# Optimization experiments

Hardware: AMD Instinct MI355X
Metric: run time of the kernel (lower is better)

Reference implementation:

```python
import jax, jax.numpy as jnp
import numpy as np
from jax import lax

B, D, BOND, OUT = 16384, 784, 5, 10

def setup_inputs() -> dict:
    key = jax.random.key(0)
    k = jax.random.split(key, 6)
    x = jax.random.uniform(k[0], (B, D), dtype=jnp.float32)
    core_first = jax.random.normal(k[1], (1, 2, BOND), dtype=jnp.float32) * 0.1
    cores_mid = jax.random.normal(k[2], (D - 2, BOND, 2, BOND), dtype=jnp.float32) * 0.1
    core_last = jax.random.normal(k[3], (BOND, 2, 1), dtype=jnp.float32) * 0.1
    # xavier_uniform for fc.weight with fan_in=1, fan_out=OUT
    bound = float(np.sqrt(6.0 / (1 + OUT)))
    fc_w = jax.random.uniform(k[4], (OUT, 1), dtype=jnp.float32, minval=-bound, maxval=bound)
    fc_b = jnp.zeros((OUT,), dtype=jnp.float32)
    return {"x": x, "core_first": core_first, "cores_mid": cores_mid,
            "core_last": core_last, "fc_w": fc_w, "fc_b": fc_b}

def reference(x, core_first, cores_mid, core_last, fc_w, fc_b):
    # x: [B, D] -> feature map [B, D, 2] = stack(1-x, x)
    xs = jnp.stack([1.0 - x, x], axis=-1)            # [B, D, 2]
    # first core: (1, 2, bond) -> initial carry [B, bond]
    carry0 = jnp.einsum('bi,ir->br', xs[:, 0], core_first[0])  # [B, bond]
    # sequential tensor-train contraction over middle sites via scan
    xs_mid = jnp.moveaxis(xs[:, 1:-1], 1, 0)          # [D-2, B, 2]
    def step(carry, inp):
        xi, core = inp                                # xi: [B,2], core: [bond,2,bond]
        carry = jnp.einsum('bl,bi,lir->br', carry, xi, core)
        return carry, None
    carry, _ = lax.scan(step, carry0, (xs_mid, cores_mid))
    # last core: (bond, 2, 1) -> scalar per batch element
    vlast = jnp.einsum('bi,li->bl', xs[:, -1], core_last[:, :, 0])  # [B, bond]
    res = jnp.sum(carry * vlast, axis=-1, keepdims=True)            # [B, 1]
    out = res @ fc_w.T + fc_b                          # [B, OUT]
    return out
```

## Files before the change

### kernel.cpp

```cpp
#include <hip/hip_runtime.h>


typedef float v4f __attribute__((ext_vector_type(4)));
typedef float v2f __attribute__((ext_vector_type(2)));

constexpr int Bn     = 16384;
constexpr int Dn     = 784;
constexpr int NOUT   = 10;
constexpr int NPAIR  = 390;
constexpr int PVEC   = 15;
constexpr int PMAT   = 12;
constexpr int RHP0   = 195;
constexpr int BWD_P0 = 375;
constexpr int PAIR_F = 100;
constexpr int WROFF  = Bn * 5;

__device__ __forceinline__ v4f splat4(float x) { v4f v = {x, x, x, x}; return v; }
__device__ __forceinline__ v4f fma4(v4f a, v4f b, v4f c) {
    return __builtin_elementwise_fma(a, b, c);
}

struct Frag { v4f r[5]; float c4[5]; };

__device__ __forceinline__ void matstepLM(const Frag& M, Frag& T,
                                          const float* __restrict__ s, v2f xc) {
    const float xa = xc[0], xb = xc[1], xab = xa * xb;
    const v4f va = splat4(xa), vb = splat4(xb), vp = splat4(xab);
    const v4f* s4 = (const v4f*)s;
#pragma unroll
    for (int l = 0; l < 5; ++l) {
        v4f crow = fma4(vp, s4[15 + l], fma4(vb, s4[10 + l], fma4(va, s4[5 + l], s4[l])));
        v4f cq = (l < 4) ? s4[20 + l] : s4[24];
        float c4l = fmaf(xab, cq[3], fmaf(xb, cq[2], fmaf(xa, cq[1], cq[0])));
#pragma unroll
        for (int i = 0; i < 5; ++i) {
            float mil = (l < 4) ? M.r[i][l] : M.c4[i];
            if (l == 0) {
                T.r[i]  = splat4(mil) * crow;
                T.c4[i] = mil * c4l;
            } else {
                T.r[i]  = fma4(splat4(mil), crow, T.r[i]);
                T.c4[i] = fmaf(mil, c4l, T.c4[i]);
            }
        }
    }
}

__device__ __forceinline__ void vecstepLM(v4f& cv, float& c4,
                                          const float* __restrict__ s, v2f xc) {
    const float xa = xc[0], xb = xc[1], xab = xa * xb;
    const v4f va = splat4(xa), vb = splat4(xb), vp = splat4(xab);
    const v4f* s4 = (const v4f*)s;
    v4f acc; float a4;
#pragma unroll
    for (int l = 0; l < 5; ++l) {
        v4f crow = fma4(vp, s4[15 + l], fma4(vb, s4[10 + l], fma4(va, s4[5 + l], s4[l])));
        v4f cq = (l < 4) ? s4[20 + l] : s4[24];
        float c4l = fmaf(xab, cq[3], fmaf(xb, cq[2], fmaf(xa, cq[1], cq[0])));
        float cl = (l < 4) ? cv[l] : c4;
        if (l == 0) { acc = splat4(cl) * crow; a4 = cl * c4l; }
        else        { acc = fma4(splat4(cl), crow, acc); a4 = fmaf(cl, c4l, a4); }
    }
    cv = acc; c4 = a4;
}

__global__ void prepack_pairs(const float* __restrict__ cm, float* __restrict__ pk)
{
    int idx = blockIdx.x * 256 + threadIdx.x;
    if (idx >= NPAIR * 100) return;
    int p = idx / 100, rest = idx - p * 100;
    int q = rest / 25, e = rest - q * 25;
    int l = e / 5, r = e - l * 5;
    int m1 = 2 * p + 1, m2 = 2 * p + 2;
    const float* L = cm + (size_t)(m1 * 5 + l) * 10;
    float acc = 0.f;
#pragma unroll
    for (int k = 0; k < 5; ++k) {
        float Lk = (q & 1) ? (L[5 + k] - L[k]) : L[k];
        const float* R = cm + (size_t)(m2 * 5 + k) * 10;
        float Rk = (q & 2) ? (R[5 + r] - R[r]) : R[r];
        acc = fmaf(Lk, Rk, acc);
    }
    int wl = l, wr = r;
    if (p >= BWD_P0) { wl = r; wr = l; }
    int off;
    if (wr < 4)      off = q * 20 + wl * 4 + wr;
    else if (wl < 4) off = 80 + wl * 4 + q;
    else             off = 96 + q;
    pk[(size_t)p * PAIR_F + off] = acc;
}

__global__ __launch_bounds__(1024, 4)
void mps_half_kernel(const float* __restrict__ x,
                     const float* __restrict__ core_first,
                     const float* __restrict__ cores_mid,
                     const float* __restrict__ core_last,
                     const float* __restrict__ pk,
                     float* __restrict__ out)
{
    __shared__ float matbuf[8][25][64];

    const int lane = threadIdx.x & 63;
    const int wave = threadIdx.x >> 6;
    const int wu   = __builtin_amdgcn_readfirstlane(wave);
    const int g    = blockIdx.x >> 1;
    const int h    = blockIdx.x & 1;
    const int row  = g * 64 + lane;
    const float* __restrict__ xr = x + (size_t)row * Dn;
    const v2f* __restrict__ xr2 = (const v2f*)xr;

    if (wu >= 1) {
        const int p0 = (h == 0 ? PVEC : RHP0) + PMAT * (wu - 1);

        Frag M, T;
        M.r[0] = {1,0,0,0}; M.r[1] = {0,1,0,0}; M.r[2] = {0,0,1,0};
        M.r[3] = {0,0,0,1}; M.r[4] = {0,0,0,0};
        M.c4[0] = 0; M.c4[1] = 0; M.c4[2] = 0; M.c4[3] = 0; M.c4[4] = 1;

        v2f x0 = xr2[p0 + 1], x1 = xr2[p0 + 2];
#pragma unroll 1
        for (int j = 0; j < PMAT; j += 2) {
            const float* s0 = pk + (size_t)(p0 + j) * PAIR_F;
            v2f nx0 = xr2[p0 + j + 3], nx1 = xr2[p0 + j + 4];
            matstepLM(M, T, s0, x0);
            matstepLM(T, M, s0 + PAIR_F, x1);
            x0 = nx0; x1 = nx1;
        }

        const bool ph1 = (h == 0) ? (wu <= 8) : (wu >= 8);
        const int  k   = (h == 0) ? (ph1 ? wu - 1 : wu - 9)
                                  : (ph1 ? 15 - wu : 7 - wu);
        if (ph1) {
#pragma unroll
            for (int i = 0; i < 5; ++i) {
#pragma unroll
                for (int r = 0; r < 4; ++r) matbuf[k][i * 5 + r][lane] = M.r[i][r];
                matbuf[k][i * 5 + 4][lane] = M.c4[i];
            }
        }
        __syncthreads();
        __syncthreads();
        if (!ph1) {
#pragma unroll
            for (int i = 0; i < 5; ++i) {
#pragma unroll
                for (int r = 0; r < 4; ++r) matbuf[k][i * 5 + r][lane] = M.r[i][r];
                matbuf[k][i * 5 + 4][lane] = M.c4[i];
            }
        }
        __syncthreads();
    } else if (h == 0) {
        v2f x01 = xr2[0];
        float cl[5], cn[5];
#pragma unroll
        for (int r = 0; r < 5; ++r)
            cl[r] = fmaf(x01[0], core_first[5 + r] - core_first[r], core_first[r]);
        const float* cm0 = cores_mid;
#pragma unroll
        for (int r = 0; r < 5; ++r) {
            float a = 0.f;
#pragma unroll
            for (int l = 0; l < 5; ++l) {
                float m = fmaf(x01[1], cm0[l * 10 + 5 + r] - cm0[l * 10 + r], cm0[l * 10 + r]);
                a = fmaf(cl[l], m, a);
            }
            cn[r] = a;
        }
        v4f cv = {cn[0], cn[1], cn[2], cn[3]};
        float c4 = cn[4];

        v2f xc = xr2[1];
#pragma unroll 1
        for (int p = 0; p < PVEC; ++p) {
            v2f nx = xr2[p + 2];
            vecstepLM(cv, c4, pk + (size_t)p * PAIR_F, xc);
            xc = nx;
        }
        cl[0] = cv[0]; cl[1] = cv[1]; cl[2] = cv[2]; cl[3] = cv[3]; cl[4] = c4;

        __syncthreads();
#pragma unroll 1
        for (int k = 0; k < 8; ++k) {
            float v0[5];
#pragma unroll
            for (int r = 0; r < 5; ++r) v0[r] = cl[0] * matbuf[k][r][lane];
#pragma unroll
            for (int l = 1; l < 5; ++l)
#pragma unroll
                for (int r = 0; r < 5; ++r)
                    v0[r] = fmaf(cl[l], matbuf[k][l * 5 + r][lane], v0[r]);
#pragma unroll
            for (int r = 0; r < 5; ++r) cl[r] = v0[r];
        }
        __syncthreads();
        __syncthreads();
#pragma unroll 1
        for (int k = 0; k < 7; ++k) {
            float v0[5];
#pragma unroll
            for (int r = 0; r < 5; ++r) v0[r] = cl[0] * matbuf[k][r][lane];
#pragma unroll
            for (int l = 1; l < 5; ++l)
#pragma unroll
                for (int r = 0; r < 5; ++r)
                    v0[r] = fmaf(cl[l], matbuf[k][l * 5 + r][lane], v0[r]);
#pragma unroll
            for (int r = 0; r < 5; ++r) cl[r] = v0[r];
        }
        float* o = out + (size_t)row * 5;
#pragma unroll
        for (int i = 0; i < 5; ++i) o[i] = cl[i];
    } else {
        v2f xz = xr2[391];
        float vl[5], vn[5];
#pragma unroll
        for (int l = 0; l < 5; ++l)
            vl[l] = fmaf(xz[1], core_last[2 * l + 1] - core_last[2 * l], core_last[2 * l]);
        const float* cmL = cores_mid + (size_t)781 * 50;
#pragma unroll
        for (int l = 0; l < 5; ++l) {
            float a = 0.f;
#pragma unroll
            for (int r = 0; r < 5; ++r) {
                float m = fmaf(xz[0], cmL[l * 10 + 5 + r] - cmL[l * 10 + r], cmL[l * 10 + r]);
                a = fmaf(m, vl[r], a);
            }
            vn[l] = a;
        }
        v4f cv = {vn[0], vn[1], vn[2], vn[3]};
        float c4 = vn[4];

        v2f xc = xr2[390];
#pragma unroll 1
        for (int p = 389; p >= BWD_P0; --p) {
            v2f nx = xr2[p];
            vecstepLM(cv, c4, pk + (size_t)p * PAIR_F, xc);
            xc = nx;
        }
        float u[5] = {cv[0], cv[1], cv[2], cv[3], c4};

        __syncthreads();
#pragma unroll 1
        for (int k = 0; k < 8; ++k) {
            float v0[5];
#pragma unroll
            for (int i = 0; i < 5; ++i) {
                float a = matbuf[k][i * 5][lane] * u[0];
#pragma unroll
                for (int l = 1; l < 5; ++l)
                    a = fmaf(matbuf[k][i * 5 + l][lane], u[l], a);
                v0[i] = a;
            }
#pragma unroll
            for (int i = 0; i < 5; ++i) u[i] = v0[i];
        }
        __syncthreads();
        __syncthreads();
#pragma unroll 1
        for (int k = 0; k < 7; ++k) {
            float v0[5];
#pragma unroll
            for (int i = 0; i < 5; ++i) {
                float a = matbuf[k][i * 5][lane] * u[0];
#pragma unroll
                for (int l = 1; l < 5; ++l)
                    a = fmaf(matbuf[k][i * 5 + l][lane], u[l], a);
                v0[i] = a;
            }
#pragma unroll
            for (int i = 0; i < 5; ++i) u[i] = v0[i];
        }
        float* o = out + WROFF + (size_t)row * 5;
#pragma unroll
        for (int i = 0; i < 5; ++i) o[i] = u[i];
    }
}

__global__ __launch_bounds__(256)
void finish_dot(const float* __restrict__ outF, float* __restrict__ res)
{
    int r = blockIdx.x * 256 + threadIdx.x;
    const float* vl = outF + (size_t)r * 5;
    const float* wr = outF + WROFF + (size_t)r * 5;
    float s = vl[0] * wr[0];
#pragma unroll
    for (int i = 1; i < 5; ++i) s = fmaf(vl[i], wr[i], s);
    res[r] = s;
}

__global__ __launch_bounds__(256)
void finish_out(const float* __restrict__ res, const float* __restrict__ fc_w,
                const float* __restrict__ fc_b, float* __restrict__ out)
{
    int r = blockIdx.x * 256 + threadIdx.x;
    float rv = res[r];
    float* o = out + (size_t)r * NOUT;
#pragma unroll
    for (int j = 0; j < NOUT; ++j) o[j] = fmaf(rv, fc_w[j], fc_b[j]);
}

extern "C" void kernel_launch(void* const* d_in, const int* in_sizes, int n_in,
                              void* d_out, int out_size, void* d_ws, size_t ws_size,
                              hipStream_t stream) {
    const float* x          = (const float*)d_in[0];
    const float* core_first = (const float*)d_in[1];
    const float* cores_mid  = (const float*)d_in[2];
    const float* core_last  = (const float*)d_in[3];
    const float* fc_w       = (const float*)d_in[4];
    const float* fc_b       = (const float*)d_in[5];
    float* out              = (float*)d_out;
    float* pk               = (float*)d_ws;
    float* res              = (float*)d_ws;

    hipLaunchKernelGGL(prepack_pairs, dim3((NPAIR * 100 + 255) / 256), dim3(256),
                       0, stream, cores_mid, pk);
    hipLaunchKernelGGL(mps_half_kernel, dim3(512), dim3(1024), 0, stream,
                       x, core_first, cores_mid, core_last, pk, out);
    hipLaunchKernelGGL(finish_dot, dim3(Bn / 256), dim3(256), 0, stream,
                       out, res);
    hipLaunchKernelGGL(finish_out, dim3(Bn / 256), dim3(256), 0, stream,
                       res, fc_w, fc_b, out);
}
```

Measured before the change: 128.9 us.

## Stage half of pair-core data in LDS and shrink matrix exchange buffer

Each block now copies the first 40 floats (the constant and xa terms) of every pair core for its half of the chain into shared memory, while the xb and xab terms are still read from global memory. The buffer used to hand 5x5 segment matrices to the vector wave shrinks from 8 to 5 slots, and the exchange becomes three phases with extra barriers. The aim is to cut global/scalar memory traffic and to use less LDS for the matrix buffer. In exchange it adds a cooperative preload with a block-wide barrier at kernel start, more synchronisation phases, and about 31 KB of extra LDS for the core copy, which may limit how many blocks fit per CU.

```diff
diff --git a/kernel.cpp b/kernel.cpp
--- a/kernel.cpp
+++ b/kernel.cpp
@@ -22,15 +22,16 @@
 
 struct Frag { v4f r[5]; float c4[5]; };
 
-__device__ __forceinline__ void matstepLM(const Frag& M, Frag& T,
-                                          const float* __restrict__ s, v2f xc) {
+__device__ __forceinline__ void matstepH(const Frag& M, Frag& T,
+                                         const v4f* __restrict__ lq,
+                                         const float* __restrict__ g, v2f xc) {
     const float xa = xc[0], xb = xc[1], xab = xa * xb;
     const v4f va = splat4(xa), vb = splat4(xb), vp = splat4(xab);
-    const v4f* s4 = (const v4f*)s;
+    const v4f* g4 = (const v4f*)g;
 #pragma unroll
     for (int l = 0; l < 5; ++l) {
-        v4f crow = fma4(vp, s4[15 + l], fma4(vb, s4[10 + l], fma4(va, s4[5 + l], s4[l])));
-        v4f cq = (l < 4) ? s4[20 + l] : s4[24];
+        v4f crow = fma4(vp, g4[5 + l], fma4(vb, g4[l], fma4(va, lq[5 + l], lq[l])));
+        v4f cq = (l < 4) ? g4[10 + l] : g4[14];
         float c4l = fmaf(xab, cq[3], fmaf(xb, cq[2], fmaf(xa, cq[1], cq[0])));
 #pragma unroll
         for (int i = 0; i < 5; ++i) {
@@ -46,16 +47,17 @@
     }
 }
 
-__device__ __forceinline__ void vecstepLM(v4f& cv, float& c4,
-                                          const float* __restrict__ s, v2f xc) {
+__device__ __forceinline__ void vecstepH(v4f& cv, float& c4,
+                                         const v4f* __restrict__ lq,
+                                         const float* __restrict__ g, v2f xc) {
     const float xa = xc[0], xb = xc[1], xab = xa * xb;
     const v4f va = splat4(xa), vb = splat4(xb), vp = splat4(xab);
-    const v4f* s4 = (const v4f*)s;
+    const v4f* g4 = (const v4f*)g;
     v4f acc; float a4;
 #pragma unroll
     for (int l = 0; l < 5; ++l) {
-        v4f crow = fma4(vp, s4[15 + l], fma4(vb, s4[10 + l], fma4(va, s4[5 + l], s4[l])));
-        v4f cq = (l < 4) ? s4[20 + l] : s4[24];
+        v4f crow = fma4(vp, g4[5 + l], fma4(vb, g4[l], fma4(va, lq[5 + l], lq[l])));
+        v4f cq = (l < 4) ? g4[10 + l] : g4[14];
         float c4l = fmaf(xab, cq[3], fmaf(xb, cq[2], fmaf(xa, cq[1], cq[0])));
         float cl = (l < 4) ? cv[l] : c4;
         if (l == 0) { acc = splat4(cl) * crow; a4 = cl * c4l; }
@@ -98,19 +100,28 @@
                      const float* __restrict__ pk,
                      float* __restrict__ out)
 {
-    __shared__ float matbuf[8][25][64];
+    __shared__ v4f   pklds[195 * 10];
+    __shared__ float matbuf[5][25][64];
 
     const int lane = threadIdx.x & 63;
     const int wave = threadIdx.x >> 6;
     const int wu   = __builtin_amdgcn_readfirstlane(wave);
     const int g    = blockIdx.x >> 1;
     const int h    = blockIdx.x & 1;
+    const int p0g  = (h == 0) ? 0 : RHP0;
     const int row  = g * 64 + lane;
     const float* __restrict__ xr = x + (size_t)row * Dn;
     const v2f* __restrict__ xr2 = (const v2f*)xr;
+    const v4f* __restrict__ pk4 = (const v4f*)pk;
+
+    for (int t = threadIdx.x; t < 195 * 10; t += 1024) {
+        int pr = t / 10, q = t - pr * 10;
+        pklds[t] = pk4[(size_t)(p0g + pr) * 25 + q];
+    }
+    __syncthreads();
 
     if (wu >= 1) {
-        const int p0 = (h == 0 ? PVEC : RHP0) + PMAT * (wu - 1);
+        const int p0 = p0g + PVEC + PMAT * (wu - 1);
 
         Frag M, T;
         M.r[0] = {1,0,0,0}; M.r[1] = {0,1,0,0}; M.r[2] = {0,0,1,0};
@@ -120,17 +131,18 @@
         v2f x0 = xr2[p0 + 1], x1 = xr2[p0 + 2];
 #pragma unroll 1
         for (int j = 0; j < PMAT; j += 2) {
-            const float* s0 = pk + (size_t)(p0 + j) * PAIR_F;
+            const v4f*  lq = pklds + (size_t)(p0 - p0g + j) * 10;
+            const float* gm = pk + (size_t)(p0 + j) * PAIR_F + 40;
             v2f nx0 = xr2[p0 + j + 3], nx1 = xr2[p0 + j + 4];
-            matstepLM(M, T, s0, x0);
-            matstepLM(T, M, s0 + PAIR_F, x1);
+            matstepH(M, T, lq, gm, x0);
+            matstepH(T, M, lq + 10, gm + PAIR_F, x1);
             x0 = nx0; x1 = nx1;
         }
 
-        const bool ph1 = (h == 0) ? (wu <= 8) : (wu >= 8);
-        const int  k   = (h == 0) ? (ph1 ? wu - 1 : wu - 9)
-                                  : (ph1 ? 15 - wu : 7 - wu);
-        if (ph1) {
+        const int ord = (h == 0) ? (wu - 1) : (15 - wu);
+        const int ph  = ord / 5;
+        const int k   = ord - ph * 5;
+        if (ph == 0) {
 #pragma unroll
             for (int i = 0; i < 5; ++i) {
 #pragma unroll
@@ -140,7 +152,17 @@
         }
         __syncthreads();
         __syncthreads();
-        if (!ph1) {
+        if (ph == 1) {
+#pragma unroll
+            for (int i = 0; i < 5; ++i) {
+#pragma unroll
+                for (int r = 0; r < 4; ++r) matbuf[k][i * 5 + r][lane] = M.r[i][r];
+                matbuf[k][i * 5 + 4][lane] = M.c4[i];
+            }
+        }
+        __syncthreads();
+        __syncthreads();
+        if (ph == 2) {
 #pragma unroll
             for (int i = 0; i < 5; ++i) {
 #pragma unroll
@@ -173,14 +195,15 @@
 #pragma unroll 1
         for (int p = 0; p < PVEC; ++p) {
             v2f nx = xr2[p + 2];
-            vecstepLM(cv, c4, pk + (size_t)p * PAIR_F, xc);
+            vecstepH(cv, c4, pklds + (size_t)p * 10,
+                     pk + (size_t)p * PAIR_F + 40, xc);
             xc = nx;
         }
         cl[0] = cv[0]; cl[1] = cv[1]; cl[2] = cv[2]; cl[3] = cv[3]; cl[4] = c4;
 
         __syncthreads();
 #pragma unroll 1
-        for (int k = 0; k < 8; ++k) {
+        for (int k = 0; k < 5; ++k) {
             float v0[5];
 #pragma unroll
             for (int r = 0; r < 5; ++r) v0[r] = cl[0] * matbuf[k][r][lane];
@@ -195,7 +218,22 @@
         __syncthreads();
         __syncthreads();
 #pragma unroll 1
-        for (int k = 0; k < 7; ++k) {
+        for (int k = 0; k < 5; ++k) {
+            float v0[5];
+#pragma unroll
+            for (int r = 0; r < 5; ++r) v0[r] = cl[0] * matbuf[k][r][lane];
+#pragma unroll
+            for (int l = 1; l < 5; ++l)
+#pragma unroll
+                for (int r = 0; r < 5; ++r)
+                    v0[r] = fmaf(cl[l], matbuf[k][l * 5 + r][lane], v0[r]);
+#pragma unroll
+            for (int r = 0; r < 5; ++r) cl[r] = v0[r];
+        }
+        __syncthreads();
+        __syncthreads();
+#pragma unroll 1
+        for (int k = 0; k < 5; ++k) {
             float v0[5];
 #pragma unroll
             for (int r = 0; r < 5; ++r) v0[r] = cl[0] * matbuf[k][r][lane];
@@ -234,14 +272,15 @@
 #pragma unroll 1
         for (int p = 389; p >= BWD_P0; --p) {
             v2f nx = xr2[p];
-            vecstepLM(cv, c4, pk + (size_t)p * PAIR_F, xc);
+            vecstepH(cv, c4, pklds + (size_t)(p - RHP0) * 10,
+                     pk + (size_t)p * PAIR_F + 40, xc);
             xc = nx;
         }
         float u[5] = {cv[0], cv[1], cv[2], cv[3], c4};
 
         __syncthreads();
 #pragma unroll 1
-        for (int k = 0; k < 8; ++k) {
+        for (int k = 0; k < 5; ++k) {
             float v0[5];
 #pragma unroll
             for (int i = 0; i < 5; ++i) {
@@ -257,7 +296,23 @@
         __syncthreads();
         __syncthreads();
 #pragma unroll 1
-        for (int k = 0; k < 7; ++k) {
+        for (int k = 0; k < 5; ++k) {
+            float v0[5];
+#pragma unroll
+            for (int i = 0; i < 5; ++i) {
+                float a = matbuf[k][i * 5][lane] * u[0];
+#pragma unroll
+                for (int l = 1; l < 5; ++l)
+                    a = fmaf(matbuf[k][i * 5 + l][lane], u[l], a);
+                v0[i] = a;
+            }
+#pragma unroll
+            for (int i = 0; i < 5; ++i) u[i] = v0[i];
+        }
+        __syncthreads();
+        __syncthreads();
+#pragma unroll 1
+        for (int k = 0; k < 5; ++k) {
             float v0[5];
 #pragma unroll
             for (int i = 0; i < 5; ++i) {
```

New measurement: 134.2 us. 4.1% more time.

## Rebalance MPS chain split: fewer waves, longer segments, single-phase matrix exchange

Applied to the files above, without the earlier changes.

The work split changes from 15 matrix waves per block-half (12 pairs each) to 7 waves of 21 pairs, with the vector waves taking 48 pairs instead of 15. The block shrinks from 1024 to 512 threads, and the two-phase shared-memory handoff with its extra barriers becomes a single write and a single barrier. A v_mov zero offset is added to the prepacked-core pointer, apparently to keep those loads from being treated as scalar-uniform. The aim is fewer barriers and less matrix-matrix overhead, at the cost of longer serial chains per wave and less parallelism per CU.

```diff
diff --git a/kernel.cpp b/kernel.cpp
--- a/kernel.cpp
+++ b/kernel.cpp
@@ -8,11 +8,11 @@
 constexpr int Dn     = 784;
 constexpr int NOUT   = 10;
 constexpr int NPAIR  = 390;
-constexpr int PVEC   = 15;
-constexpr int PMAT   = 12;
+constexpr int PAIR_F = 100;
+constexpr int LV     = 48;
+constexpr int LM     = 21;
 constexpr int RHP0   = 195;
-constexpr int BWD_P0 = 375;
-constexpr int PAIR_F = 100;
+constexpr int BWD0   = 342;
 constexpr int WROFF  = Bn * 5;
 
 __device__ __forceinline__ v4f splat4(float x) { v4f v = {x, x, x, x}; return v; }
@@ -23,7 +23,7 @@
 struct Frag { v4f r[5]; float c4[5]; };
 
 __device__ __forceinline__ void matstepLM(const Frag& M, Frag& T,
-                                          const float* __restrict__ s, v2f xc) {
+                                          const float* s, v2f xc) {
     const float xa = xc[0], xb = xc[1], xab = xa * xb;
     const v4f va = splat4(xa), vb = splat4(xb), vp = splat4(xab);
     const v4f* s4 = (const v4f*)s;
@@ -47,7 +47,7 @@
 }
 
 __device__ __forceinline__ void vecstepLM(v4f& cv, float& c4,
-                                          const float* __restrict__ s, v2f xc) {
+                                          const float* s, v2f xc) {
     const float xa = xc[0], xb = xc[1], xab = xa * xb;
     const v4f va = splat4(xa), vb = splat4(xb), vp = splat4(xab);
     const v4f* s4 = (const v4f*)s;
@@ -64,7 +64,8 @@
     cv = acc; c4 = a4;
 }
 
-__global__ void prepack_pairs(const float* __restrict__ cm, float* __restrict__ pk)
+__global__ void prepack_pairs(const float* __restrict__ cm, float* __restrict__ pk,
+                              int bwd0)
 {
     int idx = blockIdx.x * 256 + threadIdx.x;
     if (idx >= NPAIR * 100) return;
@@ -82,7 +83,7 @@
         acc = fmaf(Lk, Rk, acc);
     }
     int wl = l, wr = r;
-    if (p >= BWD_P0) { wl = r; wr = l; }
+    if (p >= bwd0) { wl = r; wr = l; }
     int off;
     if (wr < 4)      off = q * 20 + wl * 4 + wr;
     else if (wl < 4) off = 80 + wl * 4 + q;
@@ -90,7 +91,7 @@
     pk[(size_t)p * PAIR_F + off] = acc;
 }
 
-__global__ __launch_bounds__(1024, 4)
+__global__ __launch_bounds__(512, 2)
 void mps_half_kernel(const float* __restrict__ x,
                      const float* __restrict__ core_first,
                      const float* __restrict__ cores_mid,
@@ -98,7 +99,7 @@
                      const float* __restrict__ pk,
                      float* __restrict__ out)
 {
-    __shared__ float matbuf[8][25][64];
+    __shared__ float matbuf[7][25][64];
 
     const int lane = threadIdx.x & 63;
     const int wave = threadIdx.x >> 6;
@@ -106,47 +107,41 @@
     const int g    = blockIdx.x >> 1;
     const int h    = blockIdx.x & 1;
     const int row  = g * 64 + lane;
-    const float* __restrict__ xr = x + (size_t)row * Dn;
-    const v2f* __restrict__ xr2 = (const v2f*)xr;
+    const v2f* __restrict__ xr2 = (const v2f*)(x + (size_t)row * Dn);
+
+    int vzero;
+    asm volatile("v_mov_b32 %0, 0" : "=v"(vzero));
+    const float* pkv = pk + vzero;
 
     if (wu >= 1) {
-        const int p0 = (h == 0 ? PVEC : RHP0) + PMAT * (wu - 1);
+        const int p0 = (h == 0 ? LV : RHP0) + LM * (wu - 1);
 
         Frag M, T;
         M.r[0] = {1,0,0,0}; M.r[1] = {0,1,0,0}; M.r[2] = {0,0,1,0};
         M.r[3] = {0,0,0,1}; M.r[4] = {0,0,0,0};
         M.c4[0] = 0; M.c4[1] = 0; M.c4[2] = 0; M.c4[3] = 0; M.c4[4] = 1;
 
-        v2f x0 = xr2[p0 + 1], x1 = xr2[p0 + 2];
-#pragma unroll 1
-        for (int j = 0; j < PMAT; j += 2) {
-            const float* s0 = pk + (size_t)(p0 + j) * PAIR_F;
-            v2f nx0 = xr2[p0 + j + 3], nx1 = xr2[p0 + j + 4];
+        v2f x0 = xr2[p0 + 1];
+#pragma unroll 1
+        for (int j = 0; j < LM - 1; j += 2) {
+            const float* s0 = pkv + (size_t)(p0 + j) * PAIR_F;
+            v2f x1 = xr2[p0 + j + 2];
+            v2f nx0 = xr2[p0 + j + 3];
             matstepLM(M, T, s0, x0);
             matstepLM(T, M, s0 + PAIR_F, x1);
-            x0 = nx0; x1 = nx1;
-        }
-
-        const bool ph1 = (h == 0) ? (wu <= 8) : (wu >= 8);
-        const int  k   = (h == 0) ? (ph1 ? wu - 1 : wu - 9)
-                                  : (ph1 ? 15 - wu : 7 - wu);
-        if (ph1) {
-#pragma unroll
-            for (int i = 0; i < 5; ++i) {
-#pragma unroll
-                for (int r = 0; r < 4; ++r) matbuf[k][i * 5 + r][lane] = M.r[i][r];
-                matbuf[k][i * 5 + 4][lane] = M.c4[i];
-            }
-        }
-        __syncthreads();
-        __syncthreads();
-        if (!ph1) {
-#pragma unroll
-            for (int i = 0; i < 5; ++i) {
-#pragma unroll
-                for (int r = 0; r < 4; ++r) matbuf[k][i * 5 + r][lane] = M.r[i][r];
-                matbuf[k][i * 5 + 4][lane] = M.c4[i];
-            }
+            x0 = nx0;
+        }
+        {
+            matstepLM(M, T, pkv + (size_t)(p0 + LM - 1) * PAIR_F, x0);
+            M = T;
+        }
+
+        const int k = wu - 1;
+#pragma unroll
+        for (int i = 0; i < 5; ++i) {
+#pragma unroll
+            for (int r = 0; r < 4; ++r) matbuf[k][i * 5 + r][lane] = M.r[i][r];
+            matbuf[k][i * 5 + 4][lane] = M.c4[i];
         }
         __syncthreads();
     } else if (h == 0) {
@@ -171,28 +166,13 @@
 
         v2f xc = xr2[1];
 #pragma unroll 1
-        for (int p = 0; p < PVEC; ++p) {
+        for (int p = 0; p < LV; ++p) {
             v2f nx = xr2[p + 2];
-            vecstepLM(cv, c4, pk + (size_t)p * PAIR_F, xc);
+            vecstepLM(cv, c4, pkv + (size_t)p * PAIR_F, xc);
             xc = nx;
         }
         cl[0] = cv[0]; cl[1] = cv[1]; cl[2] = cv[2]; cl[3] = cv[3]; cl[4] = c4;
 
-        __syncthreads();
-#pragma unroll 1
-        for (int k = 0; k < 8; ++k) {
-            float v0[5];
-#pragma unroll
-            for (int r = 0; r < 5; ++r) v0[r] = cl[0] * matbuf[k][r][lane];
-#pragma unroll
-            for (int l = 1; l < 5; ++l)
-#pragma unroll
-                for (int r = 0; r < 5; ++r)
-                    v0[r] = fmaf(cl[l], matbuf[k][l * 5 + r][lane], v0[r]);
-#pragma unroll
-            for (int r = 0; r < 5; ++r) cl[r] = v0[r];
-        }
-        __syncthreads();
         __syncthreads();
 #pragma unroll 1
         for (int k = 0; k < 7; ++k) {
@@ -232,32 +212,16 @@
 
         v2f xc = xr2[390];
 #pragma unroll 1
-        for (int p = 389; p >= BWD_P0; --p) {
+        for (int p = 389; p >= BWD0; --p) {
             v2f nx = xr2[p];
-            vecstepLM(cv, c4, pk + (size_t)p * PAIR_F, xc);
+            vecstepLM(cv, c4, pkv + (size_t)p * PAIR_F, xc);
             xc = nx;
         }
         float u[5] = {cv[0], cv[1], cv[2], cv[3], c4};
 
         __syncthreads();
 #pragma unroll 1
-        for (int k = 0; k < 8; ++k) {
-            float v0[5];
-#pragma unroll
-            for (int i = 0; i < 5; ++i) {
-                float a = matbuf[k][i * 5][lane] * u[0];
-#pragma unroll
-                for (int l = 1; l < 5; ++l)
-                    a = fmaf(matbuf[k][i * 5 + l][lane], u[l], a);
-                v0[i] = a;
-            }
-#pragma unroll
-            for (int i = 0; i < 5; ++i) u[i] = v0[i];
-        }
-        __syncthreads();
-        __syncthreads();
-#pragma unroll 1
-        for (int k = 0; k < 7; ++k) {
+        for (int k = 6; k >= 0; --k) {
             float v0[5];
 #pragma unroll
             for (int i = 0; i < 5; ++i) {
@@ -313,8 +277,8 @@
     float* res              = (float*)d_ws;
 
     hipLaunchKernelGGL(prepack_pairs, dim3((NPAIR * 100 + 255) / 256), dim3(256),
-                       0, stream, cores_mid, pk);
-    hipLaunchKernelGGL(mps_half_kernel, dim3(512), dim3(1024), 0, stream,
+                       0, stream, cores_mid, pk, BWD0);
+    hipLaunchKernelGGL(mps_half_kernel, dim3(512), dim3(512), 0, stream,
                        x, core_first, cores_mid, core_last, pk, out);
     hipLaunchKernelGGL(finish_dot, dim3(Bn / 256), dim3(256), 0, stream,
                        out, res);
```

Result: slower. 179.0 us (+38.8%).
